# Kernel tuning notes

Hardware: AMD Instinct MI355X
Metric: run time of the kernel (lower is better)

## Reference

```python
import jax, jax.numpy as jnp
import numpy as np

N = 100000      # nodes
E = 3200000     # edges (avg degree 32)
IN, H, OUT = 20, 64, 128


def setup_inputs() -> dict:
    key = jax.random.key(0)
    ks = jax.random.split(key, 8)
    x = jax.random.normal(ks[0], (N, IN), jnp.float32)
    edge_index = jax.random.randint(ks[1], (2, E), 0, N, dtype=jnp.int32)
    # weights stored as [in, out] (transpose of torch Linear weight)
    W1 = jax.random.normal(ks[2], (IN, H), jnp.float32) / np.sqrt(IN)
    b1 = jnp.zeros((H,), jnp.float32)
    W2 = jax.random.normal(ks[3], (H, H), jnp.float32) / np.sqrt(H)
    b2 = jnp.zeros((H,), jnp.float32)
    fcW1 = jax.random.normal(ks[4], (H, H), jnp.float32) / np.sqrt(H)
    fcb1 = jnp.zeros((H,), jnp.float32)
    fcW2 = jax.random.normal(ks[5], (H, OUT), jnp.float32) / np.sqrt(H)
    fcb2 = jnp.zeros((OUT,), jnp.float32)
    return {"x": x, "edge_index": edge_index, "W1": W1, "b1": b1,
            "W2": W2, "b2": b2, "fcW1": fcW1, "fcb1": fcb1,
            "fcW2": fcW2, "fcb2": fcb2}


def _gcn_conv(x, W, b, src, dst, n):
    # GCNConv: symmetric normalization with self-loops already appended.
    h = x @ W                                                   # [N, F_out]
    deg = jax.ops.segment_sum(jnp.ones_like(dst, jnp.float32), dst,
                              num_segments=n)                   # [N]
    dinv = jnp.where(deg > 0, jax.lax.rsqrt(deg), 0.0)
    norm = dinv[src] * dinv[dst]                                # [E+N]
    agg = jax.ops.segment_sum(h[src] * norm[:, None], dst,
                              num_segments=n)                   # [N, F_out]
    return agg + b


def reference(x, edge_index, W1, b1, W2, b2, fcW1, fcb1, fcW2, fcb2):
    n = x.shape[0]
    loops = jnp.arange(n, dtype=edge_index.dtype)
    src = jnp.concatenate([edge_index[0], loops])
    dst = jnp.concatenate([edge_index[1], loops])
    h = jax.nn.relu(_gcn_conv(x, W1, b1, src, dst, n))
    h = jax.nn.relu(_gcn_conv(h, W2, b2, src, dst, n))
    g = jnp.mean(h, axis=0)                                     # [H]
    g = jax.nn.relu(g @ fcW1 + fcb1)
    return jax.nn.sigmoid(g @ fcW2 + fcb2)                      # [OUT]
```

## Files before the change

kernel.cpp:

```cpp
#include <hip/hip_runtime.h>
#include <math.h>

#define N_NODES 100000
#define HDIM 64
#define INDIM 20
#define OUTDIM 128
#define GB2 2048
#define GB2R 64
#define BSHIFT 9
#define NB 196
#define CHUNK 3072
#define CPAD 16

typedef unsigned int  u32;
typedef unsigned short u16;

__device__ __forceinline__ float4 f4add(float4 a, float4 b) {
    return make_float4(a.x + b.x, a.y + b.y, a.z + b.z, a.w + b.w);
}
__device__ __forceinline__ float bl(u32 u) {
    return __uint_as_float(u << 16);
}
__device__ __forceinline__ float bh(u32 u) {
    return __uint_as_float(u & 0xffff0000u);
}
__device__ __forceinline__ u16 f2b(float f) {
    u32 u = __float_as_uint(f);
    return (u16)((u + 0x7fffu + ((u >> 16) & 1u)) >> 16);
}

__global__ __launch_bounds__(256) void hist_kernel(const int* __restrict__ dst,
                                                   int* __restrict__ bucketCount, int E) {
    __shared__ int h[NB];
    int tid = threadIdx.x;
    for (int b = tid; b < NB; b += 256) h[b] = 0;
    __syncthreads();
    for (int e = blockIdx.x * 256 + tid; e < E; e += gridDim.x * 256)
        atomicAdd(&h[dst[e] >> BSHIFT], 1);
    __syncthreads();
    for (int b = tid; b < NB; b += 256)
        if (h[b]) atomicAdd(&bucketCount[b * CPAD], h[b]);
}

__global__ __launch_bounds__(256) void bscan_kernel(const int* __restrict__ bucketCount,
                                                    int* __restrict__ bucketBase,
                                                    int* __restrict__ bucketCursor,
                                                    int* __restrict__ rowptr, int E) {
    __shared__ int s[256];
    int tid = threadIdx.x;
    int v = (tid < NB) ? bucketCount[tid * CPAD] : 0;
    s[tid] = v;
    __syncthreads();
    for (int off = 1; off < 256; off <<= 1) {
        int t = (tid >= off) ? s[tid - off] : 0;
        __syncthreads();
        s[tid] += t;
        __syncthreads();
    }
    if (tid < NB) {
        int base = s[tid] - v;
        bucketBase[tid] = base;
        bucketCursor[tid * CPAD] = base;
    }
    if (tid == 0) { bucketBase[NB] = E; rowptr[N_NODES] = E; }
}

__global__ __launch_bounds__(256) void part_kernel(const int* __restrict__ src,
                                                   const int* __restrict__ dst,
                                                   int* __restrict__ bucketCursor,
                                                   int* __restrict__ ebuf, int E) {
    __shared__ int cnt[NB];
    __shared__ int base[NB];
    int tid = threadIdx.x;
    int e0 = blockIdx.x * CHUNK;
    int e1 = min(E, e0 + CHUNK);
    for (int b = tid; b < NB; b += 256) cnt[b] = 0;
    __syncthreads();
    for (int e = e0 + tid; e < e1; e += 256)
        atomicAdd(&cnt[dst[e] >> BSHIFT], 1);
    __syncthreads();
    for (int b = tid; b < NB; b += 256) {
        int c = cnt[b];
        base[b] = c ? atomicAdd(&bucketCursor[b * CPAD], c) : 0;
        cnt[b] = 0;
    }
    __syncthreads();
    for (int e = e0 + tid; e < e1; e += 256) {
        int d = dst[e];
        int b = d >> BSHIFT;
        int off = atomicAdd(&cnt[b], 1);
        ebuf[base[b] + off] = (src[e] << BSHIFT) | (d & ((1 << BSHIFT) - 1));
    }
}

__global__ __launch_bounds__(256) void build_kernel(const int* __restrict__ ebuf,
                                                    const int* __restrict__ bucketBase,
                                                    int* __restrict__ rowptr,
                                                    int* __restrict__ csr,
                                                    float* __restrict__ dinv, int n) {
    __shared__ int hist[512];
    __shared__ int cur[512];
    __shared__ int ps[256];
    int tid = threadIdx.x;
    int b = blockIdx.x;
    int nodeBase = b << BSHIFT;
    int ebeg = bucketBase[b], eend = bucketBase[b + 1];
    hist[tid] = 0; hist[tid + 256] = 0;
    cur[tid] = 0;  cur[tid + 256] = 0;
    __syncthreads();
    for (int e = ebeg + tid; e < eend; e += 256)
        atomicAdd(&hist[ebuf[e] & 511], 1);
    __syncthreads();
    int s0 = hist[2 * tid], s1 = hist[2 * tid + 1];
    ps[tid] = s0 + s1;
    __syncthreads();
    for (int off = 1; off < 256; off <<= 1) {
        int t = (tid >= off) ? ps[tid - off] : 0;
        __syncthreads();
        ps[tid] += t;
        __syncthreads();
    }
    int ex = ps[tid] - (s0 + s1);
    int i0 = 2 * tid, i1 = 2 * tid + 1;
    if (nodeBase + i0 < n) {
        rowptr[nodeBase + i0] = ebeg + ex;
        dinv[nodeBase + i0] = rsqrtf((float)s0 + 1.0f);
    }
    if (nodeBase + i1 < n) {
        rowptr[nodeBase + i1] = ebeg + ex + s0;
        dinv[nodeBase + i1] = rsqrtf((float)s1 + 1.0f);
    }
    hist[i0] = ex;
    hist[i1] = ex + s0;
    __syncthreads();
    for (int e = ebeg + tid; e < eend; e += 256) {
        int p = ebuf[e];
        int d = p & 511;
        int pos = hist[d] + atomicAdd(&cur[d], 1);
        csr[ebeg + pos] = p >> BSHIFT;
    }
}

__global__ __launch_bounds__(256) void xs_kernel(const float* __restrict__ x,
                                                 const float* __restrict__ dinv,
                                                 u16* __restrict__ xsb, int total) {
    int g = blockIdx.x * 256 + threadIdx.x;
    if (g < total) xsb[g] = f2b(x[g] * dinv[g / INDIM]);
}

__global__ __launch_bounds__(256) void gather1_kernel(const int* __restrict__ rowptr,
                                                      const int* __restrict__ csr,
                                                      const u16* __restrict__ xsb,
                                                      const float* __restrict__ dinv,
                                                      float* __restrict__ aggx, int n) {
    int tid = threadIdx.x;
    int w = (blockIdx.x * 256 + tid) >> 6;
    int lane = tid & 63;
    if (w >= n) return;
    int rg = lane / 5;
    int ch = lane - rg * 5;
    bool act = lane < 60;
    float4 acc = make_float4(0.f, 0.f, 0.f, 0.f);
    if (rg == 0) {
        uint2 u = *reinterpret_cast<const uint2*>(xsb + (size_t)w * INDIM + ch * 4);
        acc = make_float4(bl(u.x), bh(u.x), bl(u.y), bh(u.y));
    }
    int beg = rowptr[w], end = rowptr[w + 1];
    for (int base = beg; base < end; base += 64) {
        int cnt = min(64, end - base);
        int myi = (lane < cnt) ? csr[base + lane] : 0;
        int k = 0;
        for (; k + 12 <= cnt; k += 12) {
            int nb = __shfl(myi, k + rg);
            if (act) {
                uint2 u = *reinterpret_cast<const uint2*>(xsb + (size_t)nb * INDIM + ch * 4);
                acc = f4add(acc, make_float4(bl(u.x), bh(u.x), bl(u.y), bh(u.y)));
            }
        }
        if (k < cnt) {
            int kk = k + rg;
            if (act && kk < cnt) {
                int nb = __shfl(myi, kk);
                uint2 u = *reinterpret_cast<const uint2*>(xsb + (size_t)nb * INDIM + ch * 4);
                acc = f4add(acc, make_float4(bl(u.x), bh(u.x), bl(u.y), bh(u.y)));
            }
        }
    }
    #define F4DOWN(v, d) make_float4(__shfl_down((v).x, d), __shfl_down((v).y, d), \
                                     __shfl_down((v).z, d), __shfl_down((v).w, d))
    acc = f4add(acc, F4DOWN(acc, 30));
    acc = f4add(acc, F4DOWN(acc, 15));
    float4 a5 = F4DOWN(acc, 5);
    float4 a10 = F4DOWN(acc, 10);
    acc = f4add(f4add(acc, a5), a10);
    if (lane < 5) {
        float dw = dinv[w];
        float4 o = make_float4(acc.x * dw, acc.y * dw, acc.z * dw, acc.w * dw);
        *reinterpret_cast<float4*>(&aggx[(size_t)w * INDIM + lane * 4]) = o;
    }
}

__global__ __launch_bounds__(256) void mm12_kernel(const float* __restrict__ aggx,
                                                   const float* __restrict__ W1,
                                                   const float* __restrict__ b1,
                                                   const float* __restrict__ W2,
                                                   const float* __restrict__ dinv,
                                                   u16* __restrict__ hs2b, int n) {
    __shared__ float W1s[INDIM * HDIM];
    __shared__ float W2s[HDIM * HDIM];
    __shared__ float ax[4][INDIM];
    __shared__ float v1s[4][HDIM];
    int tid = threadIdx.x;
    for (int idx = tid; idx < INDIM * HDIM; idx += 256) W1s[idx] = W1[idx];
    for (int idx = tid; idx < HDIM * HDIM; idx += 256) W2s[idx] = W2[idx];
    int sub = tid >> 6;
    int f = tid & 63;
    int i00 = blockIdx.x * 16;
    for (int it = 0; it < 4; ++it) {
        int i0 = i00 + it * 4;
        __syncthreads();
        for (int idx = tid; idx < 4 * INDIM; idx += 256) {
            int node = i0 + idx / INDIM;
            ax[idx / INDIM][idx % INDIM] =
                (node < n) ? aggx[(size_t)node * INDIM + idx % INDIM] : 0.0f;
        }
        __syncthreads();
        float acc = b1[f];
        #pragma unroll
        for (int k = 0; k < INDIM; ++k) acc += ax[sub][k] * W1s[k * HDIM + f];
        v1s[sub][f] = fmaxf(acc, 0.0f);
        __syncthreads();
        int i = i0 + sub;
        if (i < n) {
            float acc2 = 0.0f;
            #pragma unroll
            for (int k = 0; k < HDIM; ++k) acc2 += v1s[sub][k] * W2s[k * HDIM + f];
            hs2b[(size_t)i * HDIM + f] = f2b(acc2 * dinv[i]);
        }
    }
}

#define ADD8(acc, v) do { \
    acc[0] += bl((v).x); acc[1] += bh((v).x); \
    acc[2] += bl((v).y); acc[3] += bh((v).y); \
    acc[4] += bl((v).z); acc[5] += bh((v).z); \
    acc[6] += bl((v).w); acc[7] += bh((v).w); } while (0)

__global__ __launch_bounds__(256) void gather2_kernel(const int* __restrict__ rowptr,
                                                      const int* __restrict__ csr,
                                                      const u16* __restrict__ hs2b,
                                                      const float* __restrict__ dinv,
                                                      const float* __restrict__ b2,
                                                      float* __restrict__ gpart, int n) {
    __shared__ float shp[4][64];
    int tid = threadIdx.x;
    int wv = tid >> 6;
    int lane = tid & 63;
    int rg = lane >> 3;
    int ch = lane & 7;
    float b2c[8];
    #pragma unroll
    for (int j = 0; j < 8; ++j) b2c[j] = b2[ch * 8 + j];
    float vsum[8] = {0.f, 0.f, 0.f, 0.f, 0.f, 0.f, 0.f, 0.f};
    int gw = blockIdx.x * 4 + wv;
    for (int w = gw; w < n; w += GB2 * 4) {
        float acc[8] = {0.f, 0.f, 0.f, 0.f, 0.f, 0.f, 0.f, 0.f};
        if (rg == 0) {
            uint4 v = *reinterpret_cast<const uint4*>(hs2b + (size_t)w * HDIM + ch * 8);
            ADD8(acc, v);
        }
        int beg = rowptr[w], end = rowptr[w + 1];
        for (int base = beg; base < end; base += 64) {
            int cnt = min(64, end - base);
            int myi = (lane < cnt) ? csr[base + lane] : 0;
            int k = 0;
            for (; k + 16 <= cnt; k += 16) {
                int nb0 = __shfl(myi, k + rg);
                int nb1 = __shfl(myi, k + 8 + rg);
                uint4 v0 = *reinterpret_cast<const uint4*>(hs2b + (size_t)nb0 * HDIM + ch * 8);
                uint4 v1 = *reinterpret_cast<const uint4*>(hs2b + (size_t)nb1 * HDIM + ch * 8);
                ADD8(acc, v0);
                ADD8(acc, v1);
            }
            for (; k < cnt; k += 8) {
                int kk = k + rg;
                if (kk < cnt) {
                    int nb = __shfl(myi, kk);
                    uint4 v = *reinterpret_cast<const uint4*>(hs2b + (size_t)nb * HDIM + ch * 8);
                    ADD8(acc, v);
                }
            }
        }
        #pragma unroll
        for (int j = 0; j < 8; ++j) {
            acc[j] += __shfl_xor(acc[j], 8);
            acc[j] += __shfl_xor(acc[j], 16);
            acc[j] += __shfl_xor(acc[j], 32);
        }
        float dw = dinv[w];
        #pragma unroll
        for (int j = 0; j < 8; ++j)
            vsum[j] += fmaxf(acc[j] * dw + b2c[j], 0.0f);
    }
    if (rg == 0) {
        #pragma unroll
        for (int j = 0; j < 8; ++j) shp[wv][ch * 8 + j] = vsum[j];
    }
    __syncthreads();
    if (tid < 64)
        gpart[(size_t)blockIdx.x * HDIM + tid] =
            shp[0][tid] + shp[1][tid] + shp[2][tid] + shp[3][tid];
}

__global__ __launch_bounds__(256) void reduce2_kernel(const float* __restrict__ gpart,
                                                      float* __restrict__ gpart2) {
    __shared__ float lds[256];
    int tid = threadIdx.x;
    int q = tid >> 6;
    int f = tid & 63;
    const int rows = GB2 / GB2R;
    int r0 = blockIdx.x * rows;
    float s = 0.0f;
    for (int r = r0 + q; r < r0 + rows; r += 4)
        s += gpart[(size_t)r * HDIM + f];
    lds[tid] = s;
    __syncthreads();
    if (tid < 64)
        gpart2[(size_t)blockIdx.x * HDIM + tid] =
            lds[tid] + lds[64 + tid] + lds[128 + tid] + lds[192 + tid];
}

__global__ __launch_bounds__(256) void head_kernel(const float* __restrict__ gpart2,
                                                   const float* __restrict__ fcW1,
                                                   const float* __restrict__ fcb1,
                                                   const float* __restrict__ fcW2,
                                                   const float* __restrict__ fcb2,
                                                   float* __restrict__ out, int n) {
    __shared__ float lds[256];
    __shared__ float g[HDIM];
    __shared__ float t1[HDIM];
    int tid = threadIdx.x;
    int q = tid >> 6;
    int f = tid & 63;
    float s = 0.0f;
    for (int b = q; b < GB2R; b += 4) s += gpart2[(size_t)b * HDIM + f];
    lds[tid] = s;
    __syncthreads();
    if (tid < 64)
        g[tid] = (lds[tid] + lds[64 + tid] + lds[128 + tid] + lds[192 + tid]) *
                 (1.0f / (float)n);
    __syncthreads();
    if (tid < 64) {
        float acc = fcb1[tid];
        #pragma unroll
        for (int k = 0; k < HDIM; ++k) acc += g[k] * fcW1[k * HDIM + tid];
        t1[tid] = fmaxf(acc, 0.0f);
    }
    __syncthreads();
    if (tid < OUTDIM) {
        float acc = fcb2[tid];
        #pragma unroll
        for (int j = 0; j < HDIM; ++j) acc += t1[j] * fcW2[j * OUTDIM + tid];
        out[tid] = 1.0f / (1.0f + expf(-acc));
    }
}

extern "C" void kernel_launch(void* const* d_in, const int* in_sizes, int n_in,
                              void* d_out, int out_size, void* d_ws, size_t ws_size,
                              hipStream_t stream) {
    const float* x    = (const float*)d_in[0];
    const int*   ei   = (const int*)d_in[1];
    const float* W1   = (const float*)d_in[2];
    const float* b1   = (const float*)d_in[3];
    const float* W2   = (const float*)d_in[4];
    const float* b2   = (const float*)d_in[5];
    const float* fcW1 = (const float*)d_in[6];
    const float* fcb1 = (const float*)d_in[7];
    const float* fcW2 = (const float*)d_in[8];
    const float* fcb2 = (const float*)d_in[9];
    float* out = (float*)d_out;

    const int n = N_NODES;
    const int E = in_sizes[1] / 2;
    const int* src = ei;
    const int* dst = ei + E;

    char* ws = (char*)d_ws;
    size_t off = 0;
    auto alloc = [&](size_t bytes) -> void* {
        void* p = ws + off;
        off = (off + bytes + 255) & ~(size_t)255;
        return p;
    };
    float* dinv    = (float*)alloc((size_t)n * 4);
    int*   rowptr  = (int*)  alloc((size_t)(n + 1) * 4);
    int*   bCount  = (int*)  alloc((size_t)NB * CPAD * 4);
    int*   bBase   = (int*)  alloc((NB + 1) * 4);
    int*   bCursor = (int*)  alloc((size_t)NB * CPAD * 4);
    int*   csr     = (int*)  alloc((size_t)E * 4);
    int*   ebuf    = (int*)  alloc((size_t)E * 4);
    u16*   hs2b    = (u16*)  alloc((size_t)n * HDIM * 2);
    u16*   xsb     = (u16*)  alloc((size_t)n * INDIM * 2);
    float* aggx    = (float*)alloc((size_t)n * INDIM * 4);
    float* gpart   = (float*)alloc((size_t)GB2 * HDIM * 4);
    float* gpart2  = (float*)alloc((size_t)GB2R * HDIM * 4);
    (void)ws_size;

    hipMemsetAsync(bCount, 0, (size_t)NB * CPAD * 4, stream);

    hist_kernel<<<512, 256, 0, stream>>>(dst, bCount, E);
    bscan_kernel<<<1, 256, 0, stream>>>(bCount, bBase, bCursor, rowptr, E);
    part_kernel<<<(E + CHUNK - 1) / CHUNK, 256, 0, stream>>>(src, dst, bCursor, ebuf, E);
    build_kernel<<<NB, 256, 0, stream>>>(ebuf, bBase, rowptr, csr, dinv, n);

    xs_kernel<<<(n * INDIM + 255) / 256, 256, 0, stream>>>(x, dinv, xsb, n * INDIM);

    int g1blocks = (n * 64 + 255) / 256;
    gather1_kernel<<<g1blocks, 256, 0, stream>>>(rowptr, csr, xsb, dinv, aggx, n);
    mm12_kernel<<<(n + 15) / 16, 256, 0, stream>>>(aggx, W1, b1, W2, dinv, hs2b, n);
    gather2_kernel<<<GB2, 256, 0, stream>>>(rowptr, csr, hs2b, dinv, b2, gpart, n);

    reduce2_kernel<<<GB2R, 256, 0, stream>>>(gpart, gpart2);
    head_kernel<<<1, 256, 0, stream>>>(gpart2, fcW1, fcb1, fcW2, fcb2, out, n);
}
```

Measured before the change: 361.3 us.

## Stage partitioned edges in LDS and use bf16 MFMA for second GEMM

The partition kernel now keeps each thread's edges in registers, builds per-bucket local offsets with a block scan, stages the packed edges in shared memory grouped by bucket, then writes them to the global edge buffer in contiguous runs. This replaces scattered global stores and a second read of src/dst. Separately, mm12 now handles 64 nodes per block and computes the H×H layer-2 transform with bf16 MFMA 16x16x32 instructions instead of scalar FMAs over a shared-memory W2. The trade-off is that the first-layer activations and W2 are rounded to bf16 before the matmul, which reduces precision.

```diff
diff --git a/kernel.cpp b/kernel.cpp
--- a/kernel.cpp
+++ b/kernel.cpp
@@ -10,10 +10,14 @@
 #define BSHIFT 9
 #define NB 196
 #define CHUNK 3072
+#define EPT 12
 #define CPAD 16
 
 typedef unsigned int  u32;
 typedef unsigned short u16;
+typedef unsigned char u8;
+typedef __attribute__((ext_vector_type(8))) short short8;
+typedef __attribute__((ext_vector_type(4))) float f32x4;
 
 __device__ __forceinline__ float4 f4add(float4 a, float4 b) {
     return make_float4(a.x + b.x, a.y + b.y, a.z + b.z, a.w + b.w);
@@ -70,26 +74,60 @@
                                                    int* __restrict__ bucketCursor,
                                                    int* __restrict__ ebuf, int E) {
     __shared__ int cnt[NB];
-    __shared__ int base[NB];
+    __shared__ int lofs[NB];
+    __shared__ int gbase[NB];
+    __shared__ int ps[256];
+    __shared__ int stage[CHUNK];
+    __shared__ u8  sbid[CHUNK];
     int tid = threadIdx.x;
     int e0 = blockIdx.x * CHUNK;
     int e1 = min(E, e0 + CHUNK);
     for (int b = tid; b < NB; b += 256) cnt[b] = 0;
     __syncthreads();
-    for (int e = e0 + tid; e < e1; e += 256)
-        atomicAdd(&cnt[dst[e] >> BSHIFT], 1);
-    __syncthreads();
-    for (int b = tid; b < NB; b += 256) {
-        int c = cnt[b];
-        base[b] = c ? atomicAdd(&bucketCursor[b * CPAD], c) : 0;
-        cnt[b] = 0;
-    }
-    __syncthreads();
-    for (int e = e0 + tid; e < e1; e += 256) {
-        int d = dst[e];
-        int b = d >> BSHIFT;
-        int off = atomicAdd(&cnt[b], 1);
-        ebuf[base[b] + off] = (src[e] << BSHIFT) | (d & ((1 << BSHIFT) - 1));
+    int myb[EPT];
+    int myp[EPT];
+    #pragma unroll
+    for (int j = 0; j < EPT; ++j) {
+        int e = e0 + j * 256 + tid;
+        if (e < e1) {
+            int d = dst[e];
+            int b = d >> BSHIFT;
+            myb[j] = b;
+            myp[j] = (src[e] << BSHIFT) | (d & ((1 << BSHIFT) - 1));
+            atomicAdd(&cnt[b], 1);
+        } else myb[j] = -1;
+    }
+    __syncthreads();
+    int c = (tid < NB) ? cnt[tid] : 0;
+    ps[tid] = c;
+    __syncthreads();
+    for (int off = 1; off < 256; off <<= 1) {
+        int t = (tid >= off) ? ps[tid - off] : 0;
+        __syncthreads();
+        ps[tid] += t;
+        __syncthreads();
+    }
+    if (tid < NB) {
+        lofs[tid] = ps[tid] - c;
+        gbase[tid] = c ? atomicAdd(&bucketCursor[tid * CPAD], c) : 0;
+        cnt[tid] = 0;
+    }
+    __syncthreads();
+    #pragma unroll
+    for (int j = 0; j < EPT; ++j) {
+        int b = myb[j];
+        if (b >= 0) {
+            int off = atomicAdd(&cnt[b], 1);
+            int p = lofs[b] + off;
+            stage[p] = myp[j];
+            sbid[p] = (u8)b;
+        }
+    }
+    __syncthreads();
+    int total = e1 - e0;
+    for (int i = tid; i < total; i += 256) {
+        int b = sbid[i];
+        ebuf[gbase[b] + (i - lofs[b])] = stage[i];
     }
 }
 
@@ -207,17 +245,30 @@
                                                    const float* __restrict__ dinv,
                                                    u16* __restrict__ hs2b, int n) {
     __shared__ float W1s[INDIM * HDIM];
-    __shared__ float W2s[HDIM * HDIM];
     __shared__ float ax[4][INDIM];
-    __shared__ float v1s[4][HDIM];
+    __shared__ u16 v1b[64][72];
+    __shared__ float dinvs[64];
     int tid = threadIdx.x;
     for (int idx = tid; idx < INDIM * HDIM; idx += 256) W1s[idx] = W1[idx];
-    for (int idx = tid; idx < HDIM * HDIM; idx += 256) W2s[idx] = W2[idx];
-    int sub = tid >> 6;
-    int f = tid & 63;
-    int i00 = blockIdx.x * 16;
-    for (int it = 0; it < 4; ++it) {
-        int i0 = i00 + it * 4;
+    int i00 = blockIdx.x * 64;
+    if (tid < 64) dinvs[tid] = (i00 + tid < n) ? dinv[i00 + tid] : 0.0f;
+
+    int lane = tid & 63;
+    int col = lane & 15, kq = lane >> 4;
+    short8 bfrag[2][4];
+    #pragma unroll
+    for (int kh = 0; kh < 2; ++kh)
+        #pragma unroll
+        for (int ft = 0; ft < 4; ++ft)
+            #pragma unroll
+            for (int i = 0; i < 8; ++i) {
+                int k = kh * 32 + kq * 8 + i;
+                bfrag[kh][ft][i] = (short)f2b(W2[k * HDIM + ft * 16 + col]);
+            }
+
+    int sub = tid >> 6, f = tid & 63;
+    for (int p = 0; p < 16; ++p) {
+        int i0 = i00 + p * 4;
         __syncthreads();
         for (int idx = tid; idx < 4 * INDIM; idx += 256) {
             int node = i0 + idx / INDIM;
@@ -228,14 +279,30 @@
         float acc = b1[f];
         #pragma unroll
         for (int k = 0; k < INDIM; ++k) acc += ax[sub][k] * W1s[k * HDIM + f];
-        v1s[sub][f] = fmaxf(acc, 0.0f);
-        __syncthreads();
-        int i = i0 + sub;
-        if (i < n) {
-            float acc2 = 0.0f;
-            #pragma unroll
-            for (int k = 0; k < HDIM; ++k) acc2 += v1s[sub][k] * W2s[k * HDIM + f];
-            hs2b[(size_t)i * HDIM + f] = f2b(acc2 * dinv[i]);
+        v1b[p * 4 + sub][f] = f2b(fmaxf(acc, 0.0f));
+    }
+    __syncthreads();
+
+    int wv = tid >> 6;
+    int nb0 = wv * 16;
+    short8 afrag[2];
+    #pragma unroll
+    for (int kh = 0; kh < 2; ++kh) {
+        const u16* ap = &v1b[nb0 + col][kh * 32 + kq * 8];
+        afrag[kh] = *reinterpret_cast<const short8*>(ap);
+    }
+    int gr0 = i00 + nb0;
+    #pragma unroll
+    for (int ft = 0; ft < 4; ++ft) {
+        f32x4 acc = {0.f, 0.f, 0.f, 0.f};
+        acc = __builtin_amdgcn_mfma_f32_16x16x32_bf16(afrag[0], bfrag[0][ft], acc, 0, 0, 0);
+        acc = __builtin_amdgcn_mfma_f32_16x16x32_bf16(afrag[1], bfrag[1][ft], acc, 0, 0, 0);
+        #pragma unroll
+        for (int r = 0; r < 4; ++r) {
+            int row = kq * 4 + r;
+            int node = gr0 + row;
+            if (node < n)
+                hs2b[(size_t)node * HDIM + ft * 16 + col] = f2b(acc[r] * dinvs[nb0 + row]);
         }
     }
 }
@@ -417,7 +484,7 @@
 
     int g1blocks = (n * 64 + 255) / 256;
     gather1_kernel<<<g1blocks, 256, 0, stream>>>(rowptr, csr, xsb, dinv, aggx, n);
-    mm12_kernel<<<(n + 15) / 16, 256, 0, stream>>>(aggx, W1, b1, W2, dinv, hs2b, n);
+    mm12_kernel<<<(n + 63) / 64, 256, 0, stream>>>(aggx, W1, b1, W2, dinv, hs2b, n);
     gather2_kernel<<<GB2, 256, 0, stream>>>(rowptr, csr, hs2b, dinv, b2, gpart, n);
 
     reduce2_kernel<<<GB2R, 256, 0, stream>>>(gpart, gpart2);
```

New measurement: 315.3 us. -12.7%, faster.
